# Kernel optimization log

Hardware: AMD Instinct MI355X
Metric: run time of the kernel (lower is better)

The kernel has to match this reference:

```python
import jax, jax.numpy as jnp
import numpy as np

# FlowNetC correlation config: kernel_size=1, so no kernel-window averaging;
# pad_size == max_displacement -> output spatial size == input spatial size.
B, C, H, W = 8, 256, 48, 64
MAX_DISP = 20   # max_displacement
STRIDE2 = 2     # displacement stride
PAD = 20        # pad_size
GRID_RAD = MAX_DISP // STRIDE2            # 10
GRID_W = 2 * GRID_RAD + 1                 # 21 -> 441 displacement channels


def setup_inputs() -> dict:
    key = jax.random.key(0)
    k1, k2 = jax.random.split(key)
    return {
        "input1": jax.random.normal(k1, (B, C, H, W), dtype=jnp.float32),
        "input2": jax.random.normal(k2, (B, C, H, W), dtype=jnp.float32),
    }


def _correlation(input1, input2):
    b, c, h, w = input1.shape
    p2 = jnp.pad(input2, ((0, 0), (0, 0), (PAD, PAD), (PAD, PAD)))
    # Displacement start offsets into the padded map. dy-major ordering matches
    # the CUDA kernel: top_channel = dy_idx * GRID_W + dx_idx.
    d = np.arange(-GRID_RAD, GRID_RAD + 1) * STRIDE2 + PAD  # [21]
    offs = np.stack(np.meshgrid(d, d, indexing="ij"), axis=-1).reshape(-1, 2)
    offs = jnp.asarray(offs, dtype=jnp.int32)  # [441, 2] (dy, dx)
    sumelems = jnp.float32(c)  # kernel_size^2 * C with kernel_size=1

    def step(carry, o):
        shifted = jax.lax.dynamic_slice(p2, (0, 0, o[0], o[1]), (b, c, h, w))
        # mean over channels of elementwise product -> [B, H, W]
        return carry, jnp.sum(input1 * shifted, axis=1) / sumelems

    _, ys = jax.lax.scan(step, 0, offs)          # [441, B, H, W]
    return jnp.transpose(ys, (1, 0, 2, 3))       # [B, 441, H, W]


def reference(input1, input2):
    return _correlation(input1, input2)
```

## Files before the change

kernel.cpp:

```cpp
#include <hip/hip_runtime.h>

typedef __bf16 bf16x8 __attribute__((ext_vector_type(8)));
typedef float f32x4 __attribute__((ext_vector_type(4)));
typedef unsigned short u16x8 __attribute__((ext_vector_type(8)));

#define CC 256
#define HH 48
#define WW 64
#define NB 8
#define GW 21

__global__ __launch_bounds__(256) void prep_kernel(const float* __restrict__ in1,
                                                   const float* __restrict__ in2,
                                                   unsigned short* __restrict__ o1,
                                                   unsigned short* __restrict__ o2)
{
    __shared__ float lds[CC * 33];
    int blk = blockIdx.x;
    int sel  = (blk >= 768);
    int blk2 = sel ? blk - 768 : blk;
    int b  = blk2 & 7;
    int st = blk2 >> 3;
    int s0 = st * 32;
    const float* src = sel ? in2 : in1;
    unsigned short* dst = sel ? o2 : o1;
    float scale = sel ? 1.0f : (1.0f / 256.0f);

    int t = threadIdx.x;
    int sidx = t & 31;
    int cbase = t >> 5;
    const float* sb = src + (size_t)b * CC * (HH * WW) + s0;
    #pragma unroll 4
    for (int p = 0; p < 32; ++p) {
        int c = cbase + p * 8;
        lds[c * 33 + sidx] = sb[(size_t)c * (HH * WW) + sidx] * scale;
    }
    __syncthreads();

    int cp  = t & 127;
    int sw0 = t >> 7;
    unsigned short* db = dst + ((size_t)b * (HH * WW) + s0) * CC;
    #pragma unroll 4
    for (int p = 0; p < 16; ++p) {
        int s = sw0 + p * 2;
        float f0 = lds[(2 * cp) * 33 + s];
        float f1 = lds[(2 * cp + 1) * 33 + s];
        unsigned u0 = __builtin_bit_cast(unsigned, f0);
        u0 += 0x7fffu + ((u0 >> 16) & 1u);
        unsigned u1 = __builtin_bit_cast(unsigned, f1);
        u1 += 0x7fffu + ((u1 >> 16) & 1u);
        unsigned packed = (u0 >> 16) | (u1 & 0xffff0000u);
        *(unsigned*)(db + (size_t)s * CC + 2 * cp) = packed;
    }
}

__global__ __launch_bounds__(256, 2) void corr_kernel(const unsigned short* __restrict__ in1T,
                                                      const unsigned short* __restrict__ in2T,
                                                      float* __restrict__ out)
{
    __shared__ unsigned char smem[36864];
    unsigned short* Bl = (unsigned short*)smem;

    int blk  = blockIdx.x;
    int b    = blk & 7;
    int rest = blk >> 3;
    int ysrc = (rest % 88) - 20;
    int g    = rest / 88;
    int jlo  = g * 8;
    int jhi  = (jlo + 8 < GW) ? jlo + 8 : GW;
    int tid  = threadIdx.x;

    if (ysrc < 0 || ysrc >= HH) {
        for (int j = jlo; j < jhi; ++j) {
            int yo = ysrc - 2 * (j - 10);
            if (yo < 0 || yo >= HH) continue;
            float* obase = out + (((size_t)b * 441 + (size_t)j * GW) * HH + yo) * WW;
            for (int idx = tid; idx < GW * WW; idx += 256) {
                int jx = idx >> 6;
                int x  = idx & 63;
                obase[(size_t)jx * (HH * WW) + x] = 0.0f;
            }
        }
        return;
    }

    {
        const unsigned short* b2 = in2T + ((size_t)(b * HH + ysrc) * WW) * CC;
        for (int i = tid; i < 64 * 32; i += 256) {
            int xp = i >> 5;
            int co = (i & 31) * 8;
            *(u16x8*)(Bl + xp * 264 + co) = *(const u16x8*)(b2 + (size_t)xp * CC + co);
        }
    }
    __syncthreads();

    int w    = tid >> 6;
    int lane = tid & 63;
    int l15  = lane & 15;
    int q    = lane >> 4;

    int j0 = jlo + 2 * w;
    int rv[2];
    int yout[2];
    #pragma unroll
    for (int r = 0; r < 2; ++r) {
        int j  = j0 + r;
        int yo = ysrc - 2 * (j - 10);
        rv[r]   = (j < jhi) && (yo >= 0) && (yo < HH);
        yout[r] = yo;
    }

    f32x4 acc[2][4][4];
    #pragma unroll
    for (int r = 0; r < 2; ++r)
        #pragma unroll
        for (int mt = 0; mt < 4; ++mt)
            #pragma unroll
            for (int nt = 0; nt < 4; ++nt)
                acc[r][mt][nt] = (f32x4){0.f, 0.f, 0.f, 0.f};

    const unsigned short* abase[2];
    #pragma unroll
    for (int r = 0; r < 2; ++r)
        abase[r] = rv[r]
            ? (in1T + ((size_t)((b * HH + yout[r]) * WW) + l15) * CC + q * 8)
            : in1T;

    const unsigned short* bptr = Bl + l15 * 264 + q * 8;

    for (int ks = 0; ks < 8; ++ks) {
        int c0 = ks * 32;
        bf16x8 bf[4];
        #pragma unroll
        for (int nt = 0; nt < 4; ++nt)
            bf[nt] = *(const bf16x8*)(bptr + nt * 16 * 264 + c0);
        #pragma unroll
        for (int r = 0; r < 2; ++r) {
            if (!rv[r]) continue;
            bf16x8 af[4];
            #pragma unroll
            for (int mt = 0; mt < 4; ++mt)
                af[mt] = *(const bf16x8*)(abase[r] + mt * 16 * CC + c0);
            #pragma unroll
            for (int mt = 0; mt < 4; ++mt)
                #pragma unroll
                for (int nt = 0; nt < 4; ++nt)
                    acc[r][mt][nt] = __builtin_amdgcn_mfma_f32_16x16x32_bf16(
                        af[mt], bf[nt], acc[r][mt][nt], 0, 0, 0);
        }
    }

    __syncthreads();

    float* dtw = (float*)smem + w * 2304;
    int xl  = lane & 31;
    int jxp = lane >> 5;

    #pragma unroll
    for (int r = 0; r < 2; ++r) {
        if (!rv[r]) continue;
        int j = j0 + r;
        float* orow = out + (((size_t)b * 441 + (size_t)j * GW) * HH + yout[r]) * WW;
        #pragma unroll
        for (int h = 0; h < 2; ++h) {
            #pragma unroll
            for (int mt2 = 0; mt2 < 2; ++mt2) {
                int mt = 2 * h + mt2;
                #pragma unroll
                for (int nt = 0; nt < 4; ++nt)
                    *(f32x4*)(dtw + (nt * 16 + l15) * 36 + mt2 * 16 + q * 4) = acc[r][mt][nt];
            }
            int x = h * 32 + xl;
            #pragma unroll
            for (int jj = 0; jj < 11; ++jj) {
                int jx = 2 * jj + jxp;
                if (jx >= GW) continue;
                int dx   = 2 * (jx - 10);
                int colx = x + dx;
                float v = (colx >= 0 && colx < WW) ? dtw[colx * 36 + xl] : 0.0f;
                orow[(size_t)jx * (HH * WW) + x] = v;
            }
        }
    }
}

extern "C" void kernel_launch(void* const* d_in, const int* in_sizes, int n_in,
                              void* d_out, int out_size, void* d_ws, size_t ws_size,
                              hipStream_t stream)
{
    (void)in_sizes; (void)n_in; (void)out_size; (void)ws_size;
    const float* in1 = (const float*)d_in[0];
    const float* in2 = (const float*)d_in[1];
    float* out = (float*)d_out;

    unsigned short* in1T = (unsigned short*)d_ws;
    unsigned short* in2T = in1T + (size_t)NB * HH * WW * CC;

    prep_kernel<<<dim3(1536), dim3(256), 0, stream>>>(in1, in2, in1T, in2T);
    corr_kernel<<<dim3(2112), dim3(256), 0, stream>>>(in1T, in2T, out);
}
```

Before: 131.7 us.

## Keep input2 row fragments in registers and loop all displacements per block

The correlation kernel no longer splits displacement rows into groups of 8 across blocks. Each block handles one (batch, source row) pair and loops over all 21 vertical displacements, keeping the input2 B fragments resident in registers rather than staging them through LDS. The loop also double-buffers the input1 A-fragment loads and uses nontemporal stores for the output. The prep kernel's transpose changes to scalar 16-bit stores with full unrolling. The launch drops to 704 blocks, each with much more work, and register pressure rises from holding 32 bf16x8 fragments, so occupancy and load balance may suffer.

```diff
diff --git a/kernel.cpp b/kernel.cpp
--- a/kernel.cpp
+++ b/kernel.cpp
@@ -2,11 +2,11 @@
 
 typedef __bf16 bf16x8 __attribute__((ext_vector_type(8)));
 typedef float f32x4 __attribute__((ext_vector_type(4)));
-typedef unsigned short u16x8 __attribute__((ext_vector_type(8)));
 
 #define CC 256
 #define HH 48
 #define WW 64
+#define HW (HH * WW)
 #define NB 8
 #define GW 21
 
@@ -29,28 +29,27 @@
     int t = threadIdx.x;
     int sidx = t & 31;
     int cbase = t >> 5;
-    const float* sb = src + (size_t)b * CC * (HH * WW) + s0;
-    #pragma unroll 4
+    const float* sb = src + (size_t)b * CC * HW + s0;
+    #pragma unroll
     for (int p = 0; p < 32; ++p) {
         int c = cbase + p * 8;
-        lds[c * 33 + sidx] = sb[(size_t)c * (HH * WW) + sidx] * scale;
+        lds[c * 33 + sidx] = sb[(size_t)c * HW + sidx] * scale;
     }
     __syncthreads();
 
-    int cp  = t & 127;
-    int sw0 = t >> 7;
-    unsigned short* db = dst + ((size_t)b * (HH * WW) + s0) * CC;
-    #pragma unroll 4
-    for (int p = 0; p < 16; ++p) {
-        int s = sw0 + p * 2;
-        float f0 = lds[(2 * cp) * 33 + s];
-        float f1 = lds[(2 * cp + 1) * 33 + s];
-        unsigned u0 = __builtin_bit_cast(unsigned, f0);
-        u0 += 0x7fffu + ((u0 >> 16) & 1u);
-        unsigned u1 = __builtin_bit_cast(unsigned, f1);
-        u1 += 0x7fffu + ((u1 >> 16) & 1u);
-        unsigned packed = (u0 >> 16) | (u1 & 0xffff0000u);
-        *(unsigned*)(db + (size_t)s * CC + 2 * cp) = packed;
+    int c0  = t & 63;
+    int sb2 = t >> 6;
+    unsigned short* db = dst + ((size_t)b * HW + s0) * CC;
+    #pragma unroll
+    for (int p = 0; p < 8; ++p) {
+        int s = sb2 + p * 4;
+        #pragma unroll
+        for (int ci = 0; ci < 4; ++ci) {
+            int c = c0 + 64 * ci;
+            unsigned u = __builtin_bit_cast(unsigned, lds[c * 33 + s]);
+            u += 0x7fffu + ((u >> 16) & 1u);
+            db[(size_t)s * CC + c] = (unsigned short)(u >> 16);
+        }
     }
 }
 
@@ -58,109 +57,81 @@
                                                       const unsigned short* __restrict__ in2T,
                                                       float* __restrict__ out)
 {
-    __shared__ unsigned char smem[36864];
-    unsigned short* Bl = (unsigned short*)smem;
-
+    __shared__ float dbuf[4 * 2304];
     int blk  = blockIdx.x;
     int b    = blk & 7;
-    int rest = blk >> 3;
-    int ysrc = (rest % 88) - 20;
-    int g    = rest / 88;
-    int jlo  = g * 8;
-    int jhi  = (jlo + 8 < GW) ? jlo + 8 : GW;
+    int ysrc = (blk >> 3) - 20;
     int tid  = threadIdx.x;
 
     if (ysrc < 0 || ysrc >= HH) {
-        for (int j = jlo; j < jhi; ++j) {
+        for (int j = 0; j < GW; ++j) {
             int yo = ysrc - 2 * (j - 10);
             if (yo < 0 || yo >= HH) continue;
-            float* obase = out + (((size_t)b * 441 + (size_t)j * GW) * HH + yo) * WW;
+            float* ob = out + (((size_t)b * 441 + (size_t)j * GW) * HH + yo) * WW;
             for (int idx = tid; idx < GW * WW; idx += 256) {
                 int jx = idx >> 6;
                 int x  = idx & 63;
-                obase[(size_t)jx * (HH * WW) + x] = 0.0f;
+                __builtin_nontemporal_store(0.0f, ob + (size_t)jx * HW + x);
             }
         }
         return;
     }
-
-    {
-        const unsigned short* b2 = in2T + ((size_t)(b * HH + ysrc) * WW) * CC;
-        for (int i = tid; i < 64 * 32; i += 256) {
-            int xp = i >> 5;
-            int co = (i & 31) * 8;
-            *(u16x8*)(Bl + xp * 264 + co) = *(const u16x8*)(b2 + (size_t)xp * CC + co);
-        }
-    }
-    __syncthreads();
 
     int w    = tid >> 6;
     int lane = tid & 63;
     int l15  = lane & 15;
     int q    = lane >> 4;
 
-    int j0 = jlo + 2 * w;
-    int rv[2];
-    int yout[2];
-    #pragma unroll
-    for (int r = 0; r < 2; ++r) {
-        int j  = j0 + r;
-        int yo = ysrc - 2 * (j - 10);
-        rv[r]   = (j < jhi) && (yo >= 0) && (yo < HH);
-        yout[r] = yo;
+    bf16x8 Bf[4][8];
+    {
+        const unsigned short* bl = in2T + ((size_t)(b * HH + ysrc) * WW + l15) * CC + q * 8;
+        #pragma unroll
+        for (int nt = 0; nt < 4; ++nt)
+            #pragma unroll
+            for (int ks = 0; ks < 8; ++ks)
+                Bf[nt][ks] = *(const bf16x8*)(bl + (size_t)nt * 16 * CC + ks * 32);
     }
 
-    f32x4 acc[2][4][4];
-    #pragma unroll
-    for (int r = 0; r < 2; ++r)
+    float* dtw = dbuf + w * 2304;
+    int xl  = lane & 31;
+    int jxp = lane >> 5;
+
+    for (int t = 0; t < 6; ++t) {
+        int j = w + 4 * t;
+        if (j > 20) continue;
+        int yo = ysrc - 2 * (j - 10);
+        if (yo < 0 || yo >= HH) continue;
+
+        const unsigned short* al = in1T + ((size_t)((b * HH + yo) * WW) + l15) * CC + q * 8;
+
+        f32x4 acc[4][4];
         #pragma unroll
         for (int mt = 0; mt < 4; ++mt)
             #pragma unroll
             for (int nt = 0; nt < 4; ++nt)
-                acc[r][mt][nt] = (f32x4){0.f, 0.f, 0.f, 0.f};
+                acc[mt][nt] = (f32x4){0.f, 0.f, 0.f, 0.f};
 
-    const unsigned short* abase[2];
-    #pragma unroll
-    for (int r = 0; r < 2; ++r)
-        abase[r] = rv[r]
-            ? (in1T + ((size_t)((b * HH + yout[r]) * WW) + l15) * CC + q * 8)
-            : in1T;
-
-    const unsigned short* bptr = Bl + l15 * 264 + q * 8;
-
-    for (int ks = 0; ks < 8; ++ks) {
-        int c0 = ks * 32;
-        bf16x8 bf[4];
+        bf16x8 af[2][4];
         #pragma unroll
-        for (int nt = 0; nt < 4; ++nt)
-            bf[nt] = *(const bf16x8*)(bptr + nt * 16 * 264 + c0);
+        for (int mt = 0; mt < 4; ++mt)
+            af[0][mt] = *(const bf16x8*)(al + (size_t)mt * 16 * CC);
         #pragma unroll
-        for (int r = 0; r < 2; ++r) {
-            if (!rv[r]) continue;
-            bf16x8 af[4];
-            #pragma unroll
-            for (int mt = 0; mt < 4; ++mt)
-                af[mt] = *(const bf16x8*)(abase[r] + mt * 16 * CC + c0);
+        for (int ks = 0; ks < 8; ++ks) {
+            if (ks < 7) {
+                #pragma unroll
+                for (int mt = 0; mt < 4; ++mt)
+                    af[(ks + 1) & 1][mt] =
+                        *(const bf16x8*)(al + (size_t)mt * 16 * CC + (ks + 1) * 32);
+            }
             #pragma unroll
             for (int mt = 0; mt < 4; ++mt)
                 #pragma unroll
                 for (int nt = 0; nt < 4; ++nt)
-                    acc[r][mt][nt] = __builtin_amdgcn_mfma_f32_16x16x32_bf16(
-                        af[mt], bf[nt], acc[r][mt][nt], 0, 0, 0);
+                    acc[mt][nt] = __builtin_amdgcn_mfma_f32_16x16x32_bf16(
+                        af[ks & 1][mt], Bf[nt][ks], acc[mt][nt], 0, 0, 0);
         }
-    }
 
-    __syncthreads();
-
-    float* dtw = (float*)smem + w * 2304;
-    int xl  = lane & 31;
-    int jxp = lane >> 5;
-
-    #pragma unroll
-    for (int r = 0; r < 2; ++r) {
-        if (!rv[r]) continue;
-        int j = j0 + r;
-        float* orow = out + (((size_t)b * 441 + (size_t)j * GW) * HH + yout[r]) * WW;
+        float* orow = out + (((size_t)b * 441 + (size_t)j * GW) * HH + yo) * WW;
         #pragma unroll
         for (int h = 0; h < 2; ++h) {
             #pragma unroll
@@ -168,17 +139,16 @@
                 int mt = 2 * h + mt2;
                 #pragma unroll
                 for (int nt = 0; nt < 4; ++nt)
-                    *(f32x4*)(dtw + (nt * 16 + l15) * 36 + mt2 * 16 + q * 4) = acc[r][mt][nt];
+                    *(f32x4*)(dtw + (nt * 16 + l15) * 36 + mt2 * 16 + q * 4) = acc[mt][nt];
             }
             int x = h * 32 + xl;
             #pragma unroll
             for (int jj = 0; jj < 11; ++jj) {
                 int jx = 2 * jj + jxp;
                 if (jx >= GW) continue;
-                int dx   = 2 * (jx - 10);
-                int colx = x + dx;
+                int colx = x + 2 * (jx - 10);
                 float v = (colx >= 0 && colx < WW) ? dtw[colx * 36 + xl] : 0.0f;
-                orow[(size_t)jx * (HH * WW) + x] = v;
+                __builtin_nontemporal_store(v, orow + (size_t)jx * HW + x);
             }
         }
     }
@@ -194,8 +164,8 @@
     float* out = (float*)d_out;
 
     unsigned short* in1T = (unsigned short*)d_ws;
-    unsigned short* in2T = in1T + (size_t)NB * HH * WW * CC;
+    unsigned short* in2T = in1T + (size_t)NB * HW * CC;
 
     prep_kernel<<<dim3(1536), dim3(256), 0, stream>>>(in1, in2, in1T, in2T);
-    corr_kernel<<<dim3(2112), dim3(256), 0, stream>>>(in1T, in2T, out);
+    corr_kernel<<<dim3(NB * 88), dim3(256), 0, stream>>>(in1T, in2T, out);
 }
```

New measurement: 148.0 us. 1.12x slower.
